# Kernel optimization log

Hardware: AMD Instinct MI355X
Metric: run time of the kernel (lower is better)

## Reference

```python
import jax, jax.numpy as jnp
import numpy as np

B_BOX, N_CLASS = 2, 20          # B, C from __init__
LAMBDA_C, LAMBDA_N = 5.0, 0.5   # self.lambda_c, self.lambda_n
GRID = 49                        # hard-coded 7x7 grid


def setup_inputs() -> dict:
    key = jax.random.key(0)
    k1, k2 = jax.random.split(key)
    outputs = jax.random.uniform(k1, (16384, GRID, 5 * B_BOX + N_CLASS), dtype=jnp.float32)
    target = jax.random.uniform(k2, (16384, 10, 5), dtype=jnp.float32)
    return {"outputs": outputs, "target": target}


def _forward(outputs, target):
    batch, n_obj = target.shape[0], target.shape[1]
    Bb = B_BOX
    # --- target preprocessing: sqrt(w,h), nan -> -1 ---
    tgt = target.at[:, :, 2:4].set(jnp.sqrt(target[:, :, 2:4]))
    tgt = jnp.nan_to_num(tgt, nan=-1.0)
    # --- grid-cell assignment (vectorized version of the batch*obj python loop) ---
    x, y = tgt[:, :, 0], tgt[:, :, 1]
    xi = jnp.trunc(7.0 * x).astype(jnp.int32)   # int(7*x) truncation semantics
    yi = jnp.trunc(7.0 * y).astype(jnp.int32)
    cell = jnp.clip(7 * yi + xi, 0, GRID - 1)
    valid = ((x != -1.0) & (xi >= 0)).astype(tgt.dtype)
    sel = jax.nn.one_hot(cell, GRID, dtype=tgt.dtype) * valid[..., None]   # [b,obj,49]
    ti = sel[:, :, :, None] * tgt[:, :, None, :]                           # [b,obj,49,5]
    ti = jnp.transpose(ti, (0, 2, 1, 3))                                   # [b,49,obj,5]
    # --- permute: move first Bb nonzero boxes of each cell to the top ---
    nonzero = jnp.sum(ti, axis=-1) > 0                                     # [b,49,obj]
    slot = jnp.cumsum(nonzero.astype(jnp.int32), axis=-1) - 1
    slot = jnp.where(nonzero, jnp.minimum(slot, Bb), Bb)                   # Bb = discard slot
    oh = jax.nn.one_hot(slot, Bb + 1, dtype=ti.dtype)                      # [b,49,obj,Bb+1]
    gt = jnp.einsum('bcos,bcod->bcsd', oh, ti)[:, :, :Bb]                  # [b,49,Bb,5]
    # --- iou_matrix (boxes stored as center +/- (sqrt_wh)^2 corners) ---
    pred5 = outputs[:, :, :5 * Bb].reshape(batch, GRID, Bb, 5)
    pdims = pred5[..., :4]
    pdims = pdims.at[..., 2:4].set(jnp.sqrt(pdims[..., 2:4]))
    gdims = gt[..., :4]
    gmin, gmax = gdims[..., :2] - gdims[..., 2:4] ** 2, gdims[..., :2] + gdims[..., 2:4] ** 2
    pmin, pmax = pdims[..., :2] - pdims[..., 2:4] ** 2, pdims[..., :2] + pdims[..., 2:4] ** 2
    # pairwise: axis2 = pred box, axis3 = gt box
    imin = jnp.maximum(gmin[:, :, None, :, :], pmin[:, :, :, None, :])
    imax = jnp.minimum(gmax[:, :, None, :, :], pmax[:, :, :, None, :])
    d = jnp.maximum(imax - imin, 0.0)
    inter = d[..., 0] * d[..., 1]                                          # [b,49,Bb,Bb]
    gwh, pwh = jnp.abs(gmax - gmin), jnp.abs(pmax - pmin)
    garea = (gwh[..., 0] * gwh[..., 1])[:, :, None, :]
    parea = (pwh[..., 0] * pwh[..., 1])[:, :, :, None]
    union = garea + parea - inter
    iou = jnp.where(union == 0, 0.0, inter / jnp.where(union == 0, 1.0, union))  # nan_to_num(i/u)
    t_index = jnp.argmax(iou, axis=2)                                      # [b,49,Bb]
    # --- construct_model_ground_truth: gather assigned gt box + truncated-int confidence ---
    idx = jnp.broadcast_to(t_index[..., None], gt.shape)
    gathered = jnp.take_along_axis(gt, idx, axis=2)                        # [b,49,Bb,5]
    r1wh, r2wh = pred5[..., 2:4] ** 2, gathered[..., 2:4] ** 2
    min1, max1 = pred5[..., :2] - 0.5 * r1wh, pred5[..., :2] + 0.5 * r1wh
    min2, max2 = gathered[..., :2] - 0.5 * r2wh, gathered[..., :2] + 0.5 * r2wh
    d2 = jnp.maximum(jnp.minimum(max1, max2) - jnp.maximum(min1, min2), 0.0)
    inter2 = d2[..., 0] * d2[..., 1]
    union2 = r1wh[..., 0] * r1wh[..., 1] + r2wh[..., 0] * r2wh[..., 1] - inter2
    conf = jnp.where((jnp.trunc(union2) == 0) | (jnp.trunc(inter2) == 0), 0.0,
                     jnp.trunc(inter2 / jnp.where(union2 == 0, 1.0, union2)))
    final_gt = gathered.at[..., 4].set(conf)
    # --- obj loss: lambda_c on x,y,w,h; 1.0 on confidence ---
    w = jnp.array([LAMBDA_C, LAMBDA_C, LAMBDA_C, LAMBDA_C, 1.0], dtype=outputs.dtype)
    obj_loss = jnp.sum(w * (final_gt - pred5) ** 2)
    # --- noobj loss (faithfully replicates original bug: mask is recreated per loop
    #     iteration, so only the last (batch, bbox) iteration's mask survives) ---
    pconf, gconf = pred5[..., 4], final_gt[..., 4]                         # [b,49,Bb]
    mask = jnp.ones_like(gconf)
    mask = mask.at[batch - 1, jnp.arange(GRID), t_index[batch - 1, :, Bb - 1]].set(0.0)
    noobj_loss = LAMBDA_N * jnp.sum(((pconf - gconf) * mask) ** 2)
    # --- class loss ---
    cls_scores = outputs[:, :, 5 * Bb:]                                    # [b,49,C]
    max_pred = jnp.max(cls_scores, axis=2)[..., None]                      # [b,49,1]
    pred_cls = jnp.argmax(cls_scores, axis=2)[..., None]                   # [b,49,1]
    predictions = max_pred * pconf                                         # [b,49,Bb]
    truths = (final_gt[..., 4] == pred_cls.astype(outputs.dtype)).astype(outputs.dtype)
    cell_mask = jnp.sign(jnp.sum(final_gt, axis=-1))                       # [b,49,Bb]
    class_loss = jnp.sum(cell_mask * (truths - predictions) ** 2)
    return (obj_loss + noobj_loss + class_loss) / batch


def reference(outputs, target):
    return _forward(outputs, target)
```

## Files before the change

kernel.cpp:

```cpp
#include <hip/hip_runtime.h>
#include <math.h>

#define GRID_CELLS 49
#define NOBJ 10
#define BB 2
#define NCLS 20
#define OUT_C 30
#define LAMBDA_C 5.0f
#define LAMBDA_N 0.5f
#define BLOCK 256
#define ITEMS 5
#define CELLW 11

__global__ __launch_bounds__(BLOCK) void yolo_loss_shared(
    const float* __restrict__ outputs,
    const float* __restrict__ target,
    float* __restrict__ out,
    int batch, float inv_batch)
{
    __shared__ int   cellA[ITEMS][NOBJ];
    __shared__ int   nzA[ITEMS][NOBJ];
    __shared__ float tval[ITEMS][NOBJ][5];
    __shared__ float gt[ITEMS][GRID_CELLS][CELLW];
    __shared__ float red[BLOCK / 64];

    const int t = threadIdx.x;
    const int b0 = blockIdx.x * ITEMS;

    for (int i = t; i < ITEMS * GRID_CELLS * CELLW; i += BLOCK)
        (&gt[0][0][0])[i] = 0.0f;

    if (t < ITEMS * NOBJ) {
        const int li = t / NOBJ;
        const int o  = t - li * NOBJ;
        const int b  = b0 + li;
        if (b < batch) {
            const float* tp = target + (size_t)b * (NOBJ * 5) + o * 5;
            float t0 = tp[0], t1 = tp[1];
            float t2f = sqrtf(tp[2]), t3f = sqrtf(tp[3]);
            float t4 = tp[4];
            if (t0 != t0)   t0  = -1.0f;
            if (t1 != t1)   t1  = -1.0f;
            if (t2f != t2f) t2f = -1.0f;
            if (t3f != t3f) t3f = -1.0f;
            if (t4 != t4)   t4  = -1.0f;
            int xi = (int)truncf(7.0f * t0);
            int yi = (int)truncf(7.0f * t1);
            int cell = 7 * yi + xi;
            cell = cell < 0 ? 0 : (cell > GRID_CELLS - 1 ? GRID_CELLS - 1 : cell);
            bool valid = (t0 != -1.0f) && (xi >= 0);
            float s5 = t0 + t1 + t2f + t3f + t4;
            cellA[li][o] = cell;
            nzA[li][o] = (valid && (s5 > 0.0f)) ? 1 : 0;
            tval[li][o][0] = t0; tval[li][o][1] = t1; tval[li][o][2] = t2f;
            tval[li][o][3] = t3f; tval[li][o][4] = t4;
        } else {
            nzA[li][o] = 0;
        }
    }
    __syncthreads();

    if (t < ITEMS * NOBJ) {
        const int li = t / NOBJ;
        const int o  = t - li * NOBJ;
        if (nzA[li][o]) {
            const int c = cellA[li][o];
            int slot = 0;
            for (int p = 0; p < o; ++p) slot += (nzA[li][p] && cellA[li][p] == c) ? 1 : 0;
            if (slot < BB) {
                #pragma unroll
                for (int d = 0; d < 5; ++d) gt[li][c][slot * 5 + d] = tval[li][o][d];
            }
        }
    }
    __syncthreads();

    float lsum = 0.0f;
    const int li = t / GRID_CELLS;
    const int c  = t - li * GRID_CELLS;
    const int b  = b0 + li;
    if (t < ITEMS * GRID_CELLS && b < batch) {
        float g[BB][5];
        #pragma unroll
        for (int s = 0; s < BB; ++s)
            #pragma unroll
            for (int d = 0; d < 5; ++d) g[s][d] = gt[li][c][s * 5 + d];

        const int gid = b * GRID_CELLS + c;
        const float2* r2 = reinterpret_cast<const float2*>(outputs + (size_t)gid * OUT_C);
        float pred[BB][5];
        {
            float2 p0 = r2[0], p1 = r2[1], p2 = r2[2], p3 = r2[3], p4 = r2[4];
            pred[0][0] = p0.x; pred[0][1] = p0.y; pred[0][2] = p1.x; pred[0][3] = p1.y; pred[0][4] = p2.x;
            pred[1][0] = p2.y; pred[1][1] = p3.x; pred[1][2] = p3.y; pred[1][3] = p4.x; pred[1][4] = p4.y;
        }
        float maxp; int cls;
        {
            float2 q0 = r2[5];
            maxp = q0.x; cls = 0;
            if (q0.y > maxp) { maxp = q0.y; cls = 1; }
            #pragma unroll
            for (int i = 1; i < NCLS / 2; ++i) {
                float2 q = r2[5 + i];
                if (q.x > maxp) { maxp = q.x; cls = 2 * i; }
                if (q.y > maxp) { maxp = q.y; cls = 2 * i + 1; }
            }
        }
        float fcls = (float)cls;

        float pminx[BB], pmaxx[BB], pminy[BB], pmaxy[BB], parea[BB];
        #pragma unroll
        for (int p = 0; p < BB; ++p) {
            float sw = sqrtf(pred[p][2]);
            float sh = sqrtf(pred[p][3]);
            float w2 = sw * sw, h2 = sh * sh;
            pminx[p] = pred[p][0] - w2; pmaxx[p] = pred[p][0] + w2;
            pminy[p] = pred[p][1] - h2; pmaxy[p] = pred[p][1] + h2;
            parea[p] = fabsf(pmaxx[p] - pminx[p]) * fabsf(pmaxy[p] - pminy[p]);
        }
        float gminx[BB], gmaxx[BB], gminy[BB], gmaxy[BB], garea[BB];
        #pragma unroll
        for (int s = 0; s < BB; ++s) {
            float w2 = g[s][2] * g[s][2], h2 = g[s][3] * g[s][3];
            gminx[s] = g[s][0] - w2; gmaxx[s] = g[s][0] + w2;
            gminy[s] = g[s][1] - h2; gmaxy[s] = g[s][1] + h2;
            garea[s] = fabsf(gmaxx[s] - gminx[s]) * fabsf(gmaxy[s] - gminy[s]);
        }
        int t_index[BB];
        #pragma unroll
        for (int s = 0; s < BB; ++s) {
            float best = 0.0f; int bi = 0;
            #pragma unroll
            for (int p = 0; p < BB; ++p) {
                float ix0 = fmaxf(gminx[s], pminx[p]);
                float iy0 = fmaxf(gminy[s], pminy[p]);
                float ix1 = fminf(gmaxx[s], pmaxx[p]);
                float iy1 = fminf(gmaxy[s], pmaxy[p]);
                float dx = fmaxf(ix1 - ix0, 0.0f);
                float dy = fmaxf(iy1 - iy0, 0.0f);
                float inter = dx * dy;
                float uni = garea[s] + parea[p] - inter;
                float iou = (uni == 0.0f) ? 0.0f : inter / uni;
                if (p == 0) { best = iou; bi = 0; }
                else if (iou > best) { best = iou; bi = p; }
            }
            t_index[s] = bi;
        }

        #pragma unroll
        for (int s = 0; s < BB; ++s) {
            float ga[5];
            #pragma unroll
            for (int d = 0; d < 5; ++d) ga[d] = (t_index[s] == 0) ? g[0][d] : g[1][d];
            float r1w = pred[s][2] * pred[s][2], r1h = pred[s][3] * pred[s][3];
            float r2w = ga[2] * ga[2],           r2h = ga[3] * ga[3];
            float min1x = pred[s][0] - 0.5f * r1w, max1x = pred[s][0] + 0.5f * r1w;
            float min1y = pred[s][1] - 0.5f * r1h, max1y = pred[s][1] + 0.5f * r1h;
            float min2x = ga[0] - 0.5f * r2w, max2x = ga[0] + 0.5f * r2w;
            float min2y = ga[1] - 0.5f * r2h, max2y = ga[1] + 0.5f * r2h;
            float dx = fmaxf(fminf(max1x, max2x) - fmaxf(min1x, min2x), 0.0f);
            float dy = fmaxf(fminf(max1y, max2y) - fmaxf(min1y, min2y), 0.0f);
            float inter2 = dx * dy;
            float uni2 = r1w * r1h + r2w * r2h - inter2;
            float conf;
            if (truncf(uni2) == 0.0f || truncf(inter2) == 0.0f) conf = 0.0f;
            else conf = truncf(inter2 / (uni2 == 0.0f ? 1.0f : uni2));
            #pragma unroll
            for (int d = 0; d < 4; ++d) {
                float df = ga[d] - pred[s][d];
                lsum += LAMBDA_C * df * df;
            }
            { float df = conf - pred[s][4]; lsum += df * df; }
            float m = 1.0f;
            if (b == batch - 1 && s == t_index[BB - 1]) m = 0.0f;
            float dn = (pred[s][4] - conf) * m;
            lsum += LAMBDA_N * dn * dn;
            float predn = maxp * pred[s][4];
            float truth = (conf == fcls) ? 1.0f : 0.0f;
            float sum5 = ga[0] + ga[1] + ga[2] + ga[3] + conf;
            float cm = (sum5 > 0.0f) ? 1.0f : ((sum5 < 0.0f) ? -1.0f : 0.0f);
            float dcl = truth - predn;
            lsum += cm * dcl * dcl;
        }
    }

    #pragma unroll
    for (int off = 32; off > 0; off >>= 1) lsum += __shfl_down(lsum, off, 64);
    const int wid = t >> 6;
    const int lane = t & 63;
    if (lane == 0) red[wid] = lsum;
    __syncthreads();
    if (t == 0) {
        float s = 0.0f;
        #pragma unroll
        for (int w = 0; w < BLOCK / 64; ++w) s += red[w];
        atomicAdd(out, s * inv_batch);
    }
}

extern "C" void kernel_launch(void* const* d_in, const int* in_sizes, int n_in,
                              void* d_out, int out_size, void* d_ws, size_t ws_size,
                              hipStream_t stream) {
    const float* outputs = (const float*)d_in[0];
    const float* target  = (const float*)d_in[1];
    float* out = (float*)d_out;
    int batch = in_sizes[1] / (NOBJ * 5);
    int nblocks = (batch + ITEMS - 1) / ITEMS;
    hipMemsetAsync(out, 0, sizeof(float), stream);
    yolo_loss_shared<<<nblocks, BLOCK, 0, stream>>>(outputs, target, out, batch, 1.0f / (float)batch);
}
```

Measured before the change: 161.8 us.

## Assign one wavefront per batch item with coalesced LDS staging of prediction rows

```diff
diff --git a/kernel.cpp b/kernel.cpp
--- a/kernel.cpp
+++ b/kernel.cpp
@@ -9,36 +9,51 @@
 #define LAMBDA_C 5.0f
 #define LAMBDA_N 0.5f
 #define BLOCK 256
-#define ITEMS 5
-#define CELLW 11
-
-__global__ __launch_bounds__(BLOCK) void yolo_loss_shared(
+#define WAVES (BLOCK / 64)
+#define CELLW 10
+#define ROWW (GRID_CELLS * OUT_C)
+
+__global__ __launch_bounds__(BLOCK) void yolo_loss_wave(
     const float* __restrict__ outputs,
     const float* __restrict__ target,
     float* __restrict__ out,
     int batch, float inv_batch)
 {
-    __shared__ int   cellA[ITEMS][NOBJ];
-    __shared__ int   nzA[ITEMS][NOBJ];
-    __shared__ float tval[ITEMS][NOBJ][5];
-    __shared__ float gt[ITEMS][GRID_CELLS][CELLW];
-    __shared__ float red[BLOCK / 64];
+    __shared__ __align__(16) float rows[WAVES][ROWW];
+    __shared__ float gt[WAVES][GRID_CELLS][CELLW];
+    __shared__ float red[WAVES];
 
     const int t = threadIdx.x;
-    const int b0 = blockIdx.x * ITEMS;
-
-    for (int i = t; i < ITEMS * GRID_CELLS * CELLW; i += BLOCK)
-        (&gt[0][0][0])[i] = 0.0f;
-
-    if (t < ITEMS * NOBJ) {
-        const int li = t / NOBJ;
-        const int o  = t - li * NOBJ;
-        const int b  = b0 + li;
-        if (b < batch) {
-            const float* tp = target + (size_t)b * (NOBJ * 5) + o * 5;
-            float t0 = tp[0], t1 = tp[1];
-            float t2f = sqrtf(tp[2]), t3f = sqrtf(tp[3]);
-            float t4 = tp[4];
+    const int w = t >> 6;
+    const int lane = t & 63;
+    const int b = blockIdx.x * WAVES + w;
+
+    float lsum = 0.0f;
+    if (b < batch) {
+        {
+            const float2* src = reinterpret_cast<const float2*>(outputs + (size_t)b * ROWW);
+            float2* dst = reinterpret_cast<float2*>(&rows[w][0]);
+            #pragma unroll
+            for (int i = 0; i < 12; ++i) {
+                int idx = i * 64 + lane;
+                if (idx < ROWW / 2) dst[idx] = src[idx];
+            }
+        }
+        {
+            float* gz = &gt[w][0][0];
+            #pragma unroll
+            for (int i = 0; i < 8; ++i) {
+                int idx = i * 64 + lane;
+                if (idx < GRID_CELLS * CELLW) gz[idx] = 0.0f;
+            }
+        }
+        float t0 = 0.f, t1 = 0.f, t2f = 0.f, t3f = 0.f, t4 = 0.f;
+        int cell = 0, nz = 0;
+        if (lane < NOBJ) {
+            const float* tp = target + (size_t)b * (NOBJ * 5) + lane * 5;
+            t0 = tp[0]; t1 = tp[1];
+            t2f = sqrtf(tp[2]); t3f = sqrtf(tp[3]);
+            t4 = tp[4];
             if (t0 != t0)   t0  = -1.0f;
             if (t1 != t1)   t1  = -1.0f;
             if (t2f != t2f) t2f = -1.0f;
@@ -46,154 +61,142 @@
             if (t4 != t4)   t4  = -1.0f;
             int xi = (int)truncf(7.0f * t0);
             int yi = (int)truncf(7.0f * t1);
-            int cell = 7 * yi + xi;
+            cell = 7 * yi + xi;
             cell = cell < 0 ? 0 : (cell > GRID_CELLS - 1 ? GRID_CELLS - 1 : cell);
             bool valid = (t0 != -1.0f) && (xi >= 0);
             float s5 = t0 + t1 + t2f + t3f + t4;
-            cellA[li][o] = cell;
-            nzA[li][o] = (valid && (s5 > 0.0f)) ? 1 : 0;
-            tval[li][o][0] = t0; tval[li][o][1] = t1; tval[li][o][2] = t2f;
-            tval[li][o][3] = t3f; tval[li][o][4] = t4;
-        } else {
-            nzA[li][o] = 0;
-        }
-    }
-    __syncthreads();
-
-    if (t < ITEMS * NOBJ) {
-        const int li = t / NOBJ;
-        const int o  = t - li * NOBJ;
-        if (nzA[li][o]) {
-            const int c = cellA[li][o];
-            int slot = 0;
-            for (int p = 0; p < o; ++p) slot += (nzA[li][p] && cellA[li][p] == c) ? 1 : 0;
-            if (slot < BB) {
-                #pragma unroll
-                for (int d = 0; d < 5; ++d) gt[li][c][slot * 5 + d] = tval[li][o][d];
-            }
-        }
-    }
-    __syncthreads();
-
-    float lsum = 0.0f;
-    const int li = t / GRID_CELLS;
-    const int c  = t - li * GRID_CELLS;
-    const int b  = b0 + li;
-    if (t < ITEMS * GRID_CELLS && b < batch) {
-        float g[BB][5];
+            nz = (valid && (s5 > 0.0f)) ? 1 : 0;
+        }
+        int slot = 0;
         #pragma unroll
-        for (int s = 0; s < BB; ++s)
-            #pragma unroll
-            for (int d = 0; d < 5; ++d) g[s][d] = gt[li][c][s * 5 + d];
-
-        const int gid = b * GRID_CELLS + c;
-        const float2* r2 = reinterpret_cast<const float2*>(outputs + (size_t)gid * OUT_C);
-        float pred[BB][5];
-        {
-            float2 p0 = r2[0], p1 = r2[1], p2 = r2[2], p3 = r2[3], p4 = r2[4];
-            pred[0][0] = p0.x; pred[0][1] = p0.y; pred[0][2] = p1.x; pred[0][3] = p1.y; pred[0][4] = p2.x;
-            pred[1][0] = p2.y; pred[1][1] = p3.x; pred[1][2] = p3.y; pred[1][3] = p4.x; pred[1][4] = p4.y;
-        }
-        float maxp; int cls;
-        {
-            float2 q0 = r2[5];
-            maxp = q0.x; cls = 0;
-            if (q0.y > maxp) { maxp = q0.y; cls = 1; }
-            #pragma unroll
-            for (int i = 1; i < NCLS / 2; ++i) {
-                float2 q = r2[5 + i];
-                if (q.x > maxp) { maxp = q.x; cls = 2 * i; }
-                if (q.y > maxp) { maxp = q.y; cls = 2 * i + 1; }
-            }
-        }
-        float fcls = (float)cls;
-
-        float pminx[BB], pmaxx[BB], pminy[BB], pmaxy[BB], parea[BB];
-        #pragma unroll
-        for (int p = 0; p < BB; ++p) {
-            float sw = sqrtf(pred[p][2]);
-            float sh = sqrtf(pred[p][3]);
-            float w2 = sw * sw, h2 = sh * sh;
-            pminx[p] = pred[p][0] - w2; pmaxx[p] = pred[p][0] + w2;
-            pminy[p] = pred[p][1] - h2; pmaxy[p] = pred[p][1] + h2;
-            parea[p] = fabsf(pmaxx[p] - pminx[p]) * fabsf(pmaxy[p] - pminy[p]);
-        }
-        float gminx[BB], gmaxx[BB], gminy[BB], gmaxy[BB], garea[BB];
-        #pragma unroll
-        for (int s = 0; s < BB; ++s) {
-            float w2 = g[s][2] * g[s][2], h2 = g[s][3] * g[s][3];
-            gminx[s] = g[s][0] - w2; gmaxx[s] = g[s][0] + w2;
-            gminy[s] = g[s][1] - h2; gmaxy[s] = g[s][1] + h2;
-            garea[s] = fabsf(gmaxx[s] - gminx[s]) * fabsf(gmaxy[s] - gminy[s]);
-        }
-        int t_index[BB];
-        #pragma unroll
-        for (int s = 0; s < BB; ++s) {
-            float best = 0.0f; int bi = 0;
+        for (int p = 0; p < NOBJ - 1; ++p) {
+            int cp = __shfl(cell, p, 64);
+            int np = __shfl(nz, p, 64);
+            if (p < lane && np && cp == cell) slot++;
+        }
+        if (lane < NOBJ && nz && slot < BB) {
+            gt[w][cell][slot * 5 + 0] = t0;
+            gt[w][cell][slot * 5 + 1] = t1;
+            gt[w][cell][slot * 5 + 2] = t2f;
+            gt[w][cell][slot * 5 + 3] = t3f;
+            gt[w][cell][slot * 5 + 4] = t4;
+        }
+        asm volatile("s_waitcnt lgkmcnt(0)" ::: "memory");
+
+        if (lane < GRID_CELLS) {
+            const int c = lane;
+            float g[BB][5];
+            #pragma unroll
+            for (int s = 0; s < BB; ++s)
+                #pragma unroll
+                for (int d = 0; d < 5; ++d) g[s][d] = gt[w][c][s * 5 + d];
+
+            const float2* r2 = reinterpret_cast<const float2*>(&rows[w][c * OUT_C]);
+            float pred[BB][5];
+            {
+                float2 p0 = r2[0], p1 = r2[1], p2 = r2[2], p3 = r2[3], p4 = r2[4];
+                pred[0][0] = p0.x; pred[0][1] = p0.y; pred[0][2] = p1.x; pred[0][3] = p1.y; pred[0][4] = p2.x;
+                pred[1][0] = p2.y; pred[1][1] = p3.x; pred[1][2] = p3.y; pred[1][3] = p4.x; pred[1][4] = p4.y;
+            }
+            float maxp; int cls;
+            {
+                float2 q0 = r2[5];
+                maxp = q0.x; cls = 0;
+                if (q0.y > maxp) { maxp = q0.y; cls = 1; }
+                #pragma unroll
+                for (int i = 1; i < NCLS / 2; ++i) {
+                    float2 q = r2[5 + i];
+                    if (q.x > maxp) { maxp = q.x; cls = 2 * i; }
+                    if (q.y > maxp) { maxp = q.y; cls = 2 * i + 1; }
+                }
+            }
+            float fcls = (float)cls;
+
+            float pminx[BB], pmaxx[BB], pminy[BB], pmaxy[BB], parea[BB];
             #pragma unroll
             for (int p = 0; p < BB; ++p) {
-                float ix0 = fmaxf(gminx[s], pminx[p]);
-                float iy0 = fmaxf(gminy[s], pminy[p]);
-                float ix1 = fminf(gmaxx[s], pmaxx[p]);
-                float iy1 = fminf(gmaxy[s], pmaxy[p]);
-                float dx = fmaxf(ix1 - ix0, 0.0f);
-                float dy = fmaxf(iy1 - iy0, 0.0f);
-                float inter = dx * dy;
-                float uni = garea[s] + parea[p] - inter;
-                float iou = (uni == 0.0f) ? 0.0f : inter / uni;
-                if (p == 0) { best = iou; bi = 0; }
-                else if (iou > best) { best = iou; bi = p; }
-            }
-            t_index[s] = bi;
-        }
-
-        #pragma unroll
-        for (int s = 0; s < BB; ++s) {
-            float ga[5];
-            #pragma unroll
-            for (int d = 0; d < 5; ++d) ga[d] = (t_index[s] == 0) ? g[0][d] : g[1][d];
-            float r1w = pred[s][2] * pred[s][2], r1h = pred[s][3] * pred[s][3];
-            float r2w = ga[2] * ga[2],           r2h = ga[3] * ga[3];
-            float min1x = pred[s][0] - 0.5f * r1w, max1x = pred[s][0] + 0.5f * r1w;
-            float min1y = pred[s][1] - 0.5f * r1h, max1y = pred[s][1] + 0.5f * r1h;
-            float min2x = ga[0] - 0.5f * r2w, max2x = ga[0] + 0.5f * r2w;
-            float min2y = ga[1] - 0.5f * r2h, max2y = ga[1] + 0.5f * r2h;
-            float dx = fmaxf(fminf(max1x, max2x) - fmaxf(min1x, min2x), 0.0f);
-            float dy = fmaxf(fminf(max1y, max2y) - fmaxf(min1y, min2y), 0.0f);
-            float inter2 = dx * dy;
-            float uni2 = r1w * r1h + r2w * r2h - inter2;
-            float conf;
-            if (truncf(uni2) == 0.0f || truncf(inter2) == 0.0f) conf = 0.0f;
-            else conf = truncf(inter2 / (uni2 == 0.0f ? 1.0f : uni2));
-            #pragma unroll
-            for (int d = 0; d < 4; ++d) {
-                float df = ga[d] - pred[s][d];
-                lsum += LAMBDA_C * df * df;
-            }
-            { float df = conf - pred[s][4]; lsum += df * df; }
-            float m = 1.0f;
-            if (b == batch - 1 && s == t_index[BB - 1]) m = 0.0f;
-            float dn = (pred[s][4] - conf) * m;
-            lsum += LAMBDA_N * dn * dn;
-            float predn = maxp * pred[s][4];
-            float truth = (conf == fcls) ? 1.0f : 0.0f;
-            float sum5 = ga[0] + ga[1] + ga[2] + ga[3] + conf;
-            float cm = (sum5 > 0.0f) ? 1.0f : ((sum5 < 0.0f) ? -1.0f : 0.0f);
-            float dcl = truth - predn;
-            lsum += cm * dcl * dcl;
+                float sw = sqrtf(pred[p][2]);
+                float sh = sqrtf(pred[p][3]);
+                float w2 = sw * sw, h2 = sh * sh;
+                pminx[p] = pred[p][0] - w2; pmaxx[p] = pred[p][0] + w2;
+                pminy[p] = pred[p][1] - h2; pmaxy[p] = pred[p][1] + h2;
+                parea[p] = fabsf(pmaxx[p] - pminx[p]) * fabsf(pmaxy[p] - pminy[p]);
+            }
+            float gminx[BB], gmaxx[BB], gminy[BB], gmaxy[BB], garea[BB];
+            #pragma unroll
+            for (int s = 0; s < BB; ++s) {
+                float w2 = g[s][2] * g[s][2], h2 = g[s][3] * g[s][3];
+                gminx[s] = g[s][0] - w2; gmaxx[s] = g[s][0] + w2;
+                gminy[s] = g[s][1] - h2; gmaxy[s] = g[s][1] + h2;
+                garea[s] = fabsf(gmaxx[s] - gminx[s]) * fabsf(gmaxy[s] - gminy[s]);
+            }
+            int t_index[BB];
+            #pragma unroll
+            for (int s = 0; s < BB; ++s) {
+                float best = 0.0f; int bi = 0;
+                #pragma unroll
+                for (int p = 0; p < BB; ++p) {
+                    float ix0 = fmaxf(gminx[s], pminx[p]);
+                    float iy0 = fmaxf(gminy[s], pminy[p]);
+                    float ix1 = fminf(gmaxx[s], pmaxx[p]);
+                    float iy1 = fminf(gmaxy[s], pmaxy[p]);
+                    float dx = fmaxf(ix1 - ix0, 0.0f);
+                    float dy = fmaxf(iy1 - iy0, 0.0f);
+                    float inter = dx * dy;
+                    float uni = garea[s] + parea[p] - inter;
+                    float iou = (uni == 0.0f) ? 0.0f : inter / uni;
+                    if (p == 0) { best = iou; bi = 0; }
+                    else if (iou > best) { best = iou; bi = p; }
+                }
+                t_index[s] = bi;
+            }
+
+            #pragma unroll
+            for (int s = 0; s < BB; ++s) {
+                float ga[5];
+                #pragma unroll
+                for (int d = 0; d < 5; ++d) ga[d] = (t_index[s] == 0) ? g[0][d] : g[1][d];
+                float r1w = pred[s][2] * pred[s][2], r1h = pred[s][3] * pred[s][3];
+                float r2w = ga[2] * ga[2],           r2h = ga[3] * ga[3];
+                float min1x = pred[s][0] - 0.5f * r1w, max1x = pred[s][0] + 0.5f * r1w;
+                float min1y = pred[s][1] - 0.5f * r1h, max1y = pred[s][1] + 0.5f * r1h;
+                float min2x = ga[0] - 0.5f * r2w, max2x = ga[0] + 0.5f * r2w;
+                float min2y = ga[1] - 0.5f * r2h, max2y = ga[1] + 0.5f * r2h;
+                float dx = fmaxf(fminf(max1x, max2x) - fmaxf(min1x, min2x), 0.0f);
+                float dy = fmaxf(fminf(max1y, max2y) - fmaxf(min1y, min2y), 0.0f);
+                float inter2 = dx * dy;
+                float uni2 = r1w * r1h + r2w * r2h - inter2;
+                float conf;
+                if (truncf(uni2) == 0.0f || truncf(inter2) == 0.0f) conf = 0.0f;
+                else conf = truncf(inter2 / (uni2 == 0.0f ? 1.0f : uni2));
+                #pragma unroll
+                for (int d = 0; d < 4; ++d) {
+                    float df = ga[d] - pred[s][d];
+                    lsum += LAMBDA_C * df * df;
+                }
+                { float df = conf - pred[s][4]; lsum += df * df; }
+                float m = 1.0f;
+                if (b == batch - 1 && s == t_index[BB - 1]) m = 0.0f;
+                float dn = (pred[s][4] - conf) * m;
+                lsum += LAMBDA_N * dn * dn;
+                float predn = maxp * pred[s][4];
+                float truth = (conf == fcls) ? 1.0f : 0.0f;
+                float sum5 = ga[0] + ga[1] + ga[2] + ga[3] + conf;
+                float cm = (sum5 > 0.0f) ? 1.0f : ((sum5 < 0.0f) ? -1.0f : 0.0f);
+                float dcl = truth - predn;
+                lsum += cm * dcl * dcl;
+            }
         }
     }
 
     #pragma unroll
     for (int off = 32; off > 0; off >>= 1) lsum += __shfl_down(lsum, off, 64);
-    const int wid = t >> 6;
-    const int lane = t & 63;
-    if (lane == 0) red[wid] = lsum;
+    if (lane == 0) red[w] = lsum;
     __syncthreads();
     if (t == 0) {
         float s = 0.0f;
         #pragma unroll
-        for (int w = 0; w < BLOCK / 64; ++w) s += red[w];
+        for (int v = 0; v < WAVES; ++v) s += red[v];
         atomicAdd(out, s * inv_batch);
     }
 }
@@ -205,7 +208,7 @@
     const float* target  = (const float*)d_in[1];
     float* out = (float*)d_out;
     int batch = in_sizes[1] / (NOBJ * 5);
-    int nblocks = (batch + ITEMS - 1) / ITEMS;
+    int nblocks = (batch + WAVES - 1) / WAVES;
     hipMemsetAsync(out, 0, sizeof(float), stream);
-    yolo_loss_shared<<<nblocks, BLOCK, 0, stream>>>(outputs, target, out, batch, 1.0f / (float)batch);
+    yolo_loss_wave<<<nblocks, BLOCK, 0, stream>>>(outputs, target, out, batch, 1.0f / (float)batch);
 }
```

Measured after the change: 175.1 us. 8.2% more time.
